# Optimization experiments

Hardware: AMD Instinct MI355X
Metric: run time of the kernel (lower is better)

Reference implementation:

```python
import jax, jax.numpy as jnp
import numpy as np

B, F, D_IN, H, HEADS, NC = 2048, 64, 32, 128, 4, 16
EPG = 128            # random intra-graph edges per graph
N = B * F            # 131072 nodes
E = B * EPG          # 262144 edges (self-loops added in reference, like PyG GATConv)
LRELU_ATT = 0.2      # PyG GATConv negative_slope
LRELU_CLS = 0.01     # nn.LeakyReLU default


def setup_inputs() -> dict:
    key = jax.random.key(0)
    ks = jax.random.split(key, 24)
    emb = jax.random.normal(ks[0], (B, F, D_IN), jnp.float32)
    # per-graph random connectivity, offset so graphs are disjoint
    src_l = jax.random.randint(ks[1], (B, EPG), 0, F)
    tgt_l = jax.random.randint(ks[2], (B, EPG), 0, F)
    off = (jnp.arange(B) * F)[:, None]
    edge_index = jnp.stack([(src_l + off).reshape(-1), (tgt_l + off).reshape(-1)]).astype(jnp.int32)
    batch_idx = jnp.repeat(jnp.arange(B), F).astype(jnp.int32)
    s = 0.05
    return {
        'emb': emb, 'edge_index': edge_index, 'batch_idx': batch_idx,
        # fused aligner (single unique dim 32)
        'W_align': s * jax.random.normal(ks[3], (D_IN, H), jnp.float32),
        'b_align': jnp.zeros((H,), jnp.float32),
        'gate_logits': jnp.full((F,), 2.2, jnp.float32),
        # GATConv 1: in=H, out=H per head, heads=4, concat
        'W1': s * jax.random.normal(ks[4], (H, HEADS * H), jnp.float32),
        'a_src1': s * jax.random.normal(ks[5], (HEADS, H), jnp.float32),
        'a_dst1': s * jax.random.normal(ks[6], (HEADS, H), jnp.float32),
        'b1': jnp.zeros((HEADS * H,), jnp.float32),
        # GATConv 2: in=HEADS*H, out=H, heads=1, concat=False
        'W2': s * jax.random.normal(ks[7], (HEADS * H, H), jnp.float32),
        'a_src2': s * jax.random.normal(ks[8], (1, H), jnp.float32),
        'a_dst2': s * jax.random.normal(ks[9], (1, H), jnp.float32),
        'b2': jnp.zeros((H,), jnp.float32),
        # classifier MLP
        'Wc1': s * jax.random.normal(ks[10], (H, H // 2), jnp.float32),
        'bc1': jnp.zeros((H // 2,), jnp.float32),
        'Wc2': s * jax.random.normal(ks[11], (H // 2, NC), jnp.float32),
        'bc2': jnp.zeros((NC,), jnp.float32),
    }


def gat_layer(x, src, tgt, W, a_src, a_dst, b, concat):
    heads, dout = a_src.shape
    n = x.shape[0]
    h = (x @ W).reshape(n, heads, dout)                       # [N,h,d]
    e = jax.nn.leaky_relu(jnp.einsum('nhd,hd->nh', h, a_src)[src]
                          + jnp.einsum('nhd,hd->nh', h, a_dst)[tgt], LRELU_ATT)  # [E,h]
    m = jax.ops.segment_max(e, tgt, num_segments=n)           # segment softmax over in-neighbors
    p = jnp.exp(e - m[tgt])
    ssum = jax.ops.segment_sum(p, tgt, num_segments=n)
    alpha = p / (ssum[tgt] + 1e-16)
    out = jax.ops.segment_sum(h[src] * alpha[:, :, None], tgt, num_segments=n)
    out = out.reshape(n, heads * dout) if concat else out.mean(axis=1)
    return out + b


def reference(emb, edge_index, batch_idx, W_align, b_align, gate_logits,
              W1, a_src1, a_dst1, b1, W2, a_src2, a_dst2, b2, Wc1, bc1, Wc2, bc2):
    n = emb.shape[0] * emb.shape[1]
    aligned = emb @ W_align + b_align                         # fused align: [B,F,H]
    gate = jax.nn.sigmoid(gate_logits)                        # [F]
    x = (aligned * gate[None, :, None]).reshape(n, -1)        # gated node features [N,H]
    # add self-loops (GATConv default), eval mode -> dropout is identity
    loops = jnp.arange(n, dtype=edge_index.dtype)
    src = jnp.concatenate([edge_index[0], loops])
    tgt = jnp.concatenate([edge_index[1], loops])
    x = gat_layer(x, src, tgt, W1, a_src1, a_dst1, b1, True)  # [N, 4*H]
    x = jax.nn.elu(x)
    x = gat_layer(x, src, tgt, W2, a_src2, a_dst2, b2, False) # [N, H]
    gsum = jax.ops.segment_sum(x, batch_idx, num_segments=B)  # global_mean_pool
    cnt = jax.ops.segment_sum(jnp.ones((n, 1), x.dtype), batch_idx, num_segments=B)
    g = gsum / cnt                                            # [B, H]
    hc = jax.nn.leaky_relu(g @ Wc1 + bc1, LRELU_CLS)
    logits = hc @ Wc2 + bc2                                   # [B, NC]
    return logits, gate
```

## Files before the change

kernel.cpp:

```cpp
#include <hip/hip_runtime.h>
#include <math.h>

#define BLK 256

constexpr int Bg    = 2048;
constexpr int Fn    = 64;
constexpr int DIN   = 32;
constexpr int Hd    = 128;
constexpr int HEADS = 4;
constexpr int NC    = 16;
constexpr int EPG   = 128;
constexpr int Etot  = Bg * EPG;
constexpr int W1C   = HEADS * Hd;
constexpr int NSTR  = 72;
constexpr int EROW  = 136;
constexpr int PROW  = 72;
constexpr int NE    = EPG + Fn;

typedef __attribute__((ext_vector_type(8))) __bf16 bf16x8;
typedef __attribute__((ext_vector_type(4))) __bf16 bf16x4;
typedef __attribute__((ext_vector_type(4))) float  f32x4;

__device__ __align__(16) __bf16 g_wcombT[W1C * DIN];
__device__ float g_c1[W1C];
__device__ float g_c1s[16];
__device__ __align__(16) __bf16 g_w1F[HEADS*8*64*8];
__device__ __align__(16) __bf16 g_w2F[HEADS*4*8*64*8];
__device__ __align__(16) __bf16 g_wscF[HEADS*4*64*8];
__device__ __align__(16) __bf16 g_bs1F[64*8];

__global__ __launch_bounds__(BLK) void prep1(
    const float* __restrict__ Wa, const float* __restrict__ ba,
    const float* __restrict__ W1)
{
  int i = blockIdx.x * BLK + threadIdx.x;
  if (i < DIN * W1C) {
    int k = i >> 9, n = i & 511;
    float a = 0.f;
    for (int m = 0; m < Hd; ++m) a += Wa[k*Hd + m] * W1[m*W1C + n];
    g_wcombT[n*DIN + k] = (__bf16)a;
  } else if (i < DIN*W1C + W1C) {
    int n = i - DIN*W1C;
    float a = 0.f;
    for (int m = 0; m < Hd; ++m) a += ba[m] * W1[m*W1C + n];
    g_c1[n] = a;
  }
}

constexpr int P2_W2F  = HEADS*4*8*64*8;
constexpr int P2_W1F  = HEADS*8*64*8;
constexpr int P2_WSC  = HEADS*4*64*8;
constexpr int P2_BS1  = 512;
constexpr int P2_TOT  = P2_W2F + P2_W1F + P2_WSC + P2_BS1 + 16;

__global__ __launch_bounds__(BLK) void prep2(
    const float* __restrict__ W2,
    const float* __restrict__ as1, const float* __restrict__ ad1,
    const float* __restrict__ as2, const float* __restrict__ ad2)
{
  int i = blockIdx.x * BLK + threadIdx.x;
  if (i < P2_W2F) {
    int j = i & 7, lane = (i >> 3) & 63, T = i >> 9;
    int hh = T >> 5, Ks = (T >> 3) & 3, Nt = T & 7;
    int q = lane >> 4, l = lane & 15;
    int k = hh*Hd + Ks*32 + q*8 + j;
    int n = Nt*16 + l;
    g_w2F[i] = (__bf16)W2[(size_t)k*Hd + n];
  } else if (i < P2_W2F + P2_W1F) {
    int j = i - P2_W2F;
    int jj = j & 7, lane = (j >> 3) & 63, T = j >> 9;
    int hh = T >> 3, Nt = T & 7;
    int q = lane >> 4, l = lane & 15;
    g_w1F[j] = g_wcombT[(hh*Hd + Nt*16 + l)*DIN + q*8 + jj];
  } else if (i < P2_W2F + P2_W1F + P2_WSC) {
    int j = i - (P2_W2F + P2_W1F);
    int jj = j & 7, lane = (j >> 3) & 63, T = j >> 9;
    int hh = T >> 2, Ks = T & 3;
    int q = lane >> 4, c = lane & 15;
    float a = 0.f;
    if (c < 2) {
      const float* av = c ? ad2 : as2;
      int k = hh*Hd + Ks*32 + q*8 + jj;
      for (int f = 0; f < Hd; ++f) a += W2[(size_t)k*Hd + f] * av[f];
    }
    g_wscF[j] = (__bf16)a;
  } else if (i < P2_W2F + P2_W1F + P2_WSC + P2_BS1) {
    int j = i - (P2_W2F + P2_W1F + P2_WSC);
    int jj = j & 7, lane = j >> 3;
    int q = lane >> 4, c = lane & 15;
    float a = 0.f;
    if (c < 8) {
      int h = c >> 1;
      const float* av = (c & 1) ? (ad1 + h*Hd) : (as1 + h*Hd);
      for (int f = 0; f < Hd; ++f)
        a += (float)g_wcombT[(h*Hd + f)*DIN + q*8 + jj] * av[f];
    }
    g_bs1F[j] = (__bf16)a;
  } else if (i < P2_TOT) {
    int c = i - (P2_W2F + P2_W1F + P2_WSC + P2_BS1);
    float a = 0.f;
    if (c < 8) {
      int h = c >> 1;
      const float* av = (c & 1) ? (ad1 + h*Hd) : (as1 + h*Hd);
      for (int f = 0; f < Hd; ++f) a += g_c1[h*Hd + f] * av[f];
    }
    g_c1s[c] = a;
  }
}

__global__ __launch_bounds__(BLK, 3) void gat_main(
    const float* __restrict__ emb, const int* __restrict__ ei,
    const float* __restrict__ gate_logits,
    const float* __restrict__ b1, const float* __restrict__ b2,
    const float* __restrict__ Wc1, const float* __restrict__ bc1,
    const float* __restrict__ Wc2, const float* __restrict__ bc2,
    float* __restrict__ out)
{
  __shared__ __align__(16) __bf16 hT[Hd * NSTR];
  __shared__ __align__(16) __bf16 eluS[Fn * EROW];
  __shared__ __align__(16) __bf16 Pbf[Fn * PROW];
  __shared__ float sS1s[HEADS][Fn], sS1d[HEADS][Fn];
  __shared__ float sSrc[Fn], sDst[Fn], sSum[Fn], gateS[Fn];
  __shared__ float gpool[Hd], hcS[Fn];
  __shared__ __align__(16) __bf16 wS[Fn];

  unsigned* cells = (unsigned*)eluS;

  const int b    = blockIdx.x;
  const int tid  = threadIdx.x;
  const int lane = tid & 63;
  const int wv   = tid >> 6;
  const int quad = lane >> 4;
  const int l15  = lane & 15;
  const int nodeBase = wv * 16;
  const int m0   = wv * 32;
  const int base = b * Fn;

  const f32x4 zero4 = {0.f, 0.f, 0.f, 0.f};

  int es = 0, et = 0, ecell = 0;
  if (tid < NE) {
    if (tid < EPG) {
      es = ei[(size_t)b*EPG + tid] - base;
      et = ei[(size_t)Etot + (size_t)b*EPG + tid] - base;
    } else {
      es = et = tid - EPG;
    }
    ecell = et * Fn + es;
  }
  #pragma unroll
  for (int i = 0; i < 16; ++i) cells[tid + i*BLK] = 0u;
  {
    float4* p4 = (float4*)Pbf;
    const float4 z4 = {0.f,0.f,0.f,0.f};
    p4[tid] = z4; p4[tid + 256] = z4;
    if (tid < 64) p4[tid + 512] = z4;
  }
  if (tid < Fn) {
    float g = 1.f / (1.f + expf(-gate_logits[tid]));
    gateS[tid] = g; sSum[tid] = 0.f;
    if (b == 0) out[Bg*NC + tid] = g;
  }
  bf16x8 Af;
  {
    const float* ar = emb + ((size_t)base + nodeBase + l15) * DIN + quad * 8;
    float4 e0 = *(const float4*)ar;
    float4 e1 = *(const float4*)(ar + 4);
    Af[0]=(__bf16)e0.x; Af[1]=(__bf16)e0.y; Af[2]=(__bf16)e0.z; Af[3]=(__bf16)e0.w;
    Af[4]=(__bf16)e1.x; Af[5]=(__bf16)e1.y; Af[6]=(__bf16)e1.z; Af[7]=(__bf16)e1.w;
  }
  __syncthreads();

  bool rep = false;
  if (tid < NE) rep = (atomicAdd(&cells[ecell], 1u) == 0u);
  {
    bf16x8 Bs = *(const bf16x8*)(g_bs1F + lane*8);
    f32x4 ds = __builtin_amdgcn_mfma_f32_16x16x32_bf16(Af, Bs, zero4, 0, 0, 0);
    if (l15 < 8) {
      const float cc = g_c1s[l15];
      const int h = l15 >> 1;
      float* dstArr = (l15 & 1) ? &sS1d[h][0] : &sS1s[h][0];
      #pragma unroll
      for (int r = 0; r < 4; ++r) {
        int m = nodeBase + quad*4 + r;
        dstArr[m] = gateS[m] * (ds[r] + cc);
      }
    }
  }
  __syncthreads();

  float fm = 0.f;
  if (tid < NE && rep) fm = (float)cells[ecell];

  float gq[4];
  #pragma unroll
  for (int r = 0; r < 4; ++r) gq[r] = gateS[nodeBase + quad*4 + r];

  f32x4 acc[8];
  #pragma unroll
  for (int i = 0; i < 8; ++i) acc[i] = zero4;
  f32x4 accS = zero4;

  for (int hh = 0; hh < HEADS; ++hh) {
    #pragma unroll
    for (int Nt = 0; Nt < 8; ++Nt) {
      const int n = Nt*16 + l15;
      bf16x8 Bf = *(const bf16x8*)(g_w1F + ((hh*8 + Nt)*64 + lane)*8);
      f32x4 d = __builtin_amdgcn_mfma_f32_16x16x32_bf16(Af, Bf, zero4, 0, 0, 0);
      const float c1v = g_c1[hh*Hd + n];
      bf16x4 hw;
      #pragma unroll
      for (int r = 0; r < 4; ++r) hw[r] = (__bf16)((d[r] + c1v) * gq[r]);
      *(bf16x4*)(hT + n*NSTR + nodeBase + quad*4) = hw;
    }
    if (tid < NE && rep) {
      float e = sS1s[hh][es] + sS1d[hh][et];
      e = (e > 0.f) ? e : 0.2f * e;
      float pe = fm * __expf(e);
      Pbf[et*PROW + es] = (__bf16)pe;
      atomicAdd(&sSum[et], pe);
    }
    __syncthreads();

    {
      bf16x8 Ac[2][2];
      #pragma unroll
      for (int Mi = 0; Mi < 2; ++Mi)
        #pragma unroll
        for (int Ks = 0; Ks < 2; ++Ks)
          Ac[Mi][Ks] = *(const bf16x8*)(hT + (m0 + Mi*16 + l15)*NSTR + Ks*32 + quad*8);
      float4 b1v[2];
      #pragma unroll
      for (int Mi = 0; Mi < 2; ++Mi)
        b1v[Mi] = *(const float4*)&b1[hh*Hd + m0 + Mi*16 + quad*4];
      #pragma unroll
      for (int Nt = 0; Nt < 4; ++Nt) {
        bf16x8 B0 = *(const bf16x8*)(Pbf + (Nt*16 + l15)*PROW + quad*8);
        bf16x8 B1 = *(const bf16x8*)(Pbf + (Nt*16 + l15)*PROW + 32 + quad*8);
        const int t = Nt*16 + l15;
        const float si = 1.f / (sSum[t] + 1e-16f);
        #pragma unroll
        for (int Mi = 0; Mi < 2; ++Mi) {
          f32x4 d = __builtin_amdgcn_mfma_f32_16x16x32_bf16(Ac[Mi][0], B0, zero4, 0, 0, 0);
          d = __builtin_amdgcn_mfma_f32_16x16x32_bf16(Ac[Mi][1], B1, d, 0, 0, 0);
          bf16x4 w;
          #pragma unroll
          for (int r = 0; r < 4; ++r) {
            float hv = d[r]*si + b1v[Mi][r];
            hv = (hv > 0.f) ? hv : (__expf(hv) - 1.f);
            w[r] = (__bf16)hv;
          }
          *(bf16x4*)(eluS + t*EROW + m0 + Mi*16 + quad*4) = w;
        }
      }
    }
    __syncthreads();

    #pragma unroll
    for (int Ks = 0; Ks < 4; ++Ks) {
      bf16x8 A2 = *(const bf16x8*)(eluS + (nodeBase + l15)*EROW + Ks*32 + quad*8);
      #pragma unroll
      for (int Nt = 0; Nt < 8; ++Nt) {
        bf16x8 B2 = *(const bf16x8*)(g_w2F + (((hh*4 + Ks)*8 + Nt)*64 + lane)*8);
        acc[Nt] = __builtin_amdgcn_mfma_f32_16x16x32_bf16(A2, B2, acc[Nt], 0, 0, 0);
      }
      bf16x8 Bs2 = *(const bf16x8*)(g_wscF + ((hh*4 + Ks)*64 + lane)*8);
      accS = __builtin_amdgcn_mfma_f32_16x16x32_bf16(A2, Bs2, accS, 0, 0, 0);
    }
    {
      float4* p4 = (float4*)Pbf;
      const float4 z4 = {0.f,0.f,0.f,0.f};
      p4[tid] = z4; p4[tid + 256] = z4;
      if (tid < 64) p4[tid + 512] = z4;
      if (tid < Fn) sSum[tid] = 0.f;
    }
    __syncthreads();
  }

  #pragma unroll
  for (int Nt = 0; Nt < 8; ++Nt) {
    const int n = Nt*16 + l15;
    bf16x4 hw;
    #pragma unroll
    for (int r = 0; r < 4; ++r) hw[r] = (__bf16)acc[Nt][r];
    *(bf16x4*)(hT + n*NSTR + nodeBase + quad*4) = hw;
  }
  if (l15 == 0) {
    #pragma unroll
    for (int r = 0; r < 4; ++r) sSrc[nodeBase + quad*4 + r] = accS[r];
  } else if (l15 == 1) {
    #pragma unroll
    for (int r = 0; r < 4; ++r) sDst[nodeBase + quad*4 + r] = accS[r];
  }
  __syncthreads();

  if (tid < NE && rep) {
    float e = sSrc[es] + sDst[et];
    e = (e > 0.f) ? e : 0.2f * e;
    float pe = fm * __expf(e);
    Pbf[et*PROW + es] = (__bf16)pe;
    atomicAdd(&sSum[et], pe);
  }
  __syncthreads();

  {
    const int s_ = tid >> 2, part = tid & 3;
    float a = 0.f;
    #pragma unroll
    for (int q = 0; q < 16; ++q) {
      const int t = part*16 + q;
      a += (1.f / (sSum[t] + 1e-16f)) * (float)Pbf[t*PROW + s_];
    }
    a += __shfl_xor(a, 1);
    a += __shfl_xor(a, 2);
    if (part == 0) wS[s_] = (__bf16)(a * (1.f/64.f));
  }
  __syncthreads();

  {
    #pragma unroll
    for (int Mi = 0; Mi < 2; ++Mi) {
      f32x4 d = zero4;
      #pragma unroll
      for (int Ks = 0; Ks < 2; ++Ks) {
        bf16x8 A = *(const bf16x8*)(hT + (m0 + Mi*16 + l15)*NSTR + Ks*32 + quad*8);
        bf16x8 Bw = *(const bf16x8*)(wS + Ks*32 + quad*8);
        d = __builtin_amdgcn_mfma_f32_16x16x32_bf16(A, Bw, d, 0, 0, 0);
      }
      if (l15 == 0) {
        #pragma unroll
        for (int r = 0; r < 4; ++r) {
          const int f = m0 + Mi*16 + quad*4 + r;
          gpool[f] = d[r] + b2[f];
        }
      }
    }
  }
  __syncthreads();

  {
    const int c = tid >> 2, p = tid & 3;
    float a = 0.f;
    #pragma unroll
    for (int i = 0; i < 32; ++i) {
      const int k = p*32 + i;
      a += gpool[k] * Wc1[k*Fn + c];
    }
    a += __shfl_xor(a, 1);
    a += __shfl_xor(a, 2);
    if (p == 0) {
      a += bc1[c];
      hcS[c] = (a > 0.f) ? a : 0.01f * a;
    }
  }
  __syncthreads();

  {
    const int c = tid >> 4, p = tid & 15;
    float a = 0.f;
    #pragma unroll
    for (int i = 0; i < 4; ++i) {
      const int k = p*4 + i;
      a += hcS[k] * Wc2[k*NC + c];
    }
    a += __shfl_xor(a, 1);
    a += __shfl_xor(a, 2);
    a += __shfl_xor(a, 4);
    a += __shfl_xor(a, 8);
    if (p == 0) out[b*NC + c] = a + bc2[c];
  }
}

extern "C" void kernel_launch(void* const* d_in, const int* in_sizes, int n_in,
                              void* d_out, int out_size, void* d_ws, size_t ws_size,
                              hipStream_t stream) {
  const float* emb = (const float*)d_in[0];
  const int*   ei  = (const int*)  d_in[1];
  const float* Wa  = (const float*)d_in[3];
  const float* ba  = (const float*)d_in[4];
  const float* gl  = (const float*)d_in[5];
  const float* W1  = (const float*)d_in[6];
  const float* as1 = (const float*)d_in[7];
  const float* ad1 = (const float*)d_in[8];
  const float* b1  = (const float*)d_in[9];
  const float* W2  = (const float*)d_in[10];
  const float* as2 = (const float*)d_in[11];
  const float* ad2 = (const float*)d_in[12];
  const float* b2  = (const float*)d_in[13];
  const float* Wc1 = (const float*)d_in[14];
  const float* bc1 = (const float*)d_in[15];
  const float* Wc2 = (const float*)d_in[16];
  const float* bc2 = (const float*)d_in[17];
  float* out = (float*)d_out;

  const int prep1N = DIN*W1C + W1C;
  hipLaunchKernelGGL(prep1, dim3((prep1N + BLK - 1)/BLK), dim3(BLK), 0, stream,
                     Wa, ba, W1);
  hipLaunchKernelGGL(prep2, dim3((P2_TOT + BLK - 1)/BLK), dim3(BLK), 0, stream,
                     W2, as1, ad1, as2, ad2);
  hipLaunchKernelGGL(gat_main, dim3(Bg), dim3(BLK), 0, stream,
                     emb, ei, gl, b1, b2, Wc1, bc1, Wc2, bc2, out);
}
```

Measured before the change: 197.1 us.

## Shrink LDS row strides and parallelize weight-prep kernels with coalesced loads

Reduces the hT and Pbf row padding from 72 to 68 bf16, which shrinks shared memory per block and changes the LDS bank mapping for the MFMA operand reads. The prep kernels are restructured. prep1 stages W_align in LDS and writes coalesced output. prep2 scatters W2 from coalesced reads, and splits the attention-projection dot products across lanes with shuffle reductions and unrolled partial sums. The smaller stride may raise occupancy or cut bank conflicts, but 16-byte vector loads at stride 68 need alignment care. The prep kernels are a small part of total time.

```diff
diff --git a/kernel.cpp b/kernel.cpp
--- a/kernel.cpp
+++ b/kernel.cpp
@@ -12,9 +12,9 @@
 constexpr int EPG   = 128;
 constexpr int Etot  = Bg * EPG;
 constexpr int W1C   = HEADS * Hd;
-constexpr int NSTR  = 72;
+constexpr int NSTR  = 68;
 constexpr int EROW  = 136;
-constexpr int PROW  = 72;
+constexpr int PROW  = 68;
 constexpr int NE    = EPG + Fn;
 
 typedef __attribute__((ext_vector_type(8))) __bf16 bf16x8;
@@ -33,25 +33,54 @@
     const float* __restrict__ Wa, const float* __restrict__ ba,
     const float* __restrict__ W1)
 {
-  int i = blockIdx.x * BLK + threadIdx.x;
+  __shared__ float WaS[DIN * Hd];
+  const int tid = threadIdx.x;
+  for (int i = tid; i < DIN * Hd; i += BLK) {
+    int k = i >> 7, m = i & 127;
+    WaS[m * DIN + k] = Wa[i];
+  }
+  __syncthreads();
+
+  int i = blockIdx.x * BLK + tid;
   if (i < DIN * W1C) {
-    int k = i >> 9, n = i & 511;
-    float a = 0.f;
-    for (int m = 0; m < Hd; ++m) a += Wa[k*Hd + m] * W1[m*W1C + n];
-    g_wcombT[n*DIN + k] = (__bf16)a;
+    int k = i & 31, n = i >> 5;
+    float a0 = 0.f, a1 = 0.f, a2 = 0.f, a3 = 0.f;
+    #pragma unroll
+    for (int m = 0; m < Hd; m += 4) {
+      a0 += WaS[(m  )*DIN + k] * W1[(m  )*W1C + n];
+      a1 += WaS[(m+1)*DIN + k] * W1[(m+1)*W1C + n];
+      a2 += WaS[(m+2)*DIN + k] * W1[(m+2)*W1C + n];
+      a3 += WaS[(m+3)*DIN + k] * W1[(m+3)*W1C + n];
+    }
+    g_wcombT[i] = (__bf16)(a0 + a1 + a2 + a3);
   } else if (i < DIN*W1C + W1C) {
     int n = i - DIN*W1C;
-    float a = 0.f;
-    for (int m = 0; m < Hd; ++m) a += ba[m] * W1[m*W1C + n];
-    g_c1[n] = a;
+    float a0 = 0.f, a1 = 0.f, a2 = 0.f, a3 = 0.f;
+    #pragma unroll
+    for (int m = 0; m < Hd; m += 4) {
+      a0 += ba[m  ] * W1[(m  )*W1C + n];
+      a1 += ba[m+1] * W1[(m+1)*W1C + n];
+      a2 += ba[m+2] * W1[(m+2)*W1C + n];
+      a3 += ba[m+3] * W1[(m+3)*W1C + n];
+    }
+    g_c1[n] = a0 + a1 + a2 + a3;
   }
 }
 
-constexpr int P2_W2F  = HEADS*4*8*64*8;
-constexpr int P2_W1F  = HEADS*8*64*8;
-constexpr int P2_WSC  = HEADS*4*64*8;
-constexpr int P2_BS1  = 512;
-constexpr int P2_TOT  = P2_W2F + P2_W1F + P2_WSC + P2_BS1 + 16;
+constexpr int R_W2F  = 65536;
+constexpr int R_W1F  = 16384;
+constexpr int R_WSCZ = 8192;
+constexpr int R_WSCD = 4096;
+constexpr int R_BS1Z = 512;
+constexpr int R_BS1D = 1024;
+constexpr int R_C1S  = 128;
+constexpr int B0 = R_W2F;
+constexpr int B1 = B0 + R_W1F;
+constexpr int B2 = B1 + R_WSCZ;
+constexpr int B3 = B2 + R_WSCD;
+constexpr int B4 = B3 + R_BS1Z;
+constexpr int B5 = B4 + R_BS1D;
+constexpr int P2_TOT = B5 + R_C1S;
 
 __global__ __launch_bounds__(BLK) void prep2(
     const float* __restrict__ W2,
@@ -59,52 +88,84 @@
     const float* __restrict__ as2, const float* __restrict__ ad2)
 {
   int i = blockIdx.x * BLK + threadIdx.x;
-  if (i < P2_W2F) {
-    int j = i & 7, lane = (i >> 3) & 63, T = i >> 9;
-    int hh = T >> 5, Ks = (T >> 3) & 3, Nt = T & 7;
-    int q = lane >> 4, l = lane & 15;
-    int k = hh*Hd + Ks*32 + q*8 + j;
-    int n = Nt*16 + l;
-    g_w2F[i] = (__bf16)W2[(size_t)k*Hd + n];
-  } else if (i < P2_W2F + P2_W1F) {
-    int j = i - P2_W2F;
+  if (i < B0) {
+    int k = i >> 7, n = i & 127;
+    int hh = k >> 7, Ks = (k >> 5) & 3, q = (k >> 3) & 3, j = k & 7;
+    int Nt = n >> 4, l = n & 15;
+    int idx = (((hh*4 + Ks)*8 + Nt)*64 + (q*16 + l))*8 + j;
+    g_w2F[idx] = (__bf16)W2[i];
+  } else if (i < B1) {
+    int j = i - B0;
     int jj = j & 7, lane = (j >> 3) & 63, T = j >> 9;
     int hh = T >> 3, Nt = T & 7;
     int q = lane >> 4, l = lane & 15;
     g_w1F[j] = g_wcombT[(hh*Hd + Nt*16 + l)*DIN + q*8 + jj];
-  } else if (i < P2_W2F + P2_W1F + P2_WSC) {
-    int j = i - (P2_W2F + P2_W1F);
-    int jj = j & 7, lane = (j >> 3) & 63, T = j >> 9;
-    int hh = T >> 2, Ks = T & 3;
-    int q = lane >> 4, c = lane & 15;
-    float a = 0.f;
-    if (c < 2) {
-      const float* av = c ? ad2 : as2;
-      int k = hh*Hd + Ks*32 + q*8 + jj;
-      for (int f = 0; f < Hd; ++f) a += W2[(size_t)k*Hd + f] * av[f];
-    }
-    g_wscF[j] = (__bf16)a;
-  } else if (i < P2_W2F + P2_W1F + P2_WSC + P2_BS1) {
-    int j = i - (P2_W2F + P2_W1F + P2_WSC);
-    int jj = j & 7, lane = j >> 3;
-    int q = lane >> 4, c = lane & 15;
+  } else if (i < B2) {
+    int j = i - B1;
+    int lane = (j >> 3) & 63, c = lane & 15;
+    if (c >= 2) g_wscF[j] = (__bf16)0.f;
+  } else if (i < B3) {
+    int j = i - B2;
+    int p = j & 3, c = (j >> 2) & 1, k = j >> 3;
+    const float* av = c ? ad2 : as2;
+    float a0 = 0.f, a1 = 0.f, a2 = 0.f, a3 = 0.f;
+    #pragma unroll
+    for (int q = 0; q < 32; q += 4) {
+      int f = p*32 + q;
+      a0 += W2[(size_t)k*Hd + f    ] * av[f    ];
+      a1 += W2[(size_t)k*Hd + f + 1] * av[f + 1];
+      a2 += W2[(size_t)k*Hd + f + 2] * av[f + 2];
+      a3 += W2[(size_t)k*Hd + f + 3] * av[f + 3];
+    }
+    float a = a0 + a1 + a2 + a3;
+    a += __shfl_xor(a, 1);
+    a += __shfl_xor(a, 2);
+    if (p == 0) {
+      int T = k >> 5, q2 = (k >> 3) & 3, jj = k & 7;
+      g_wscF[(T*64 + q2*16 + c)*8 + jj] = (__bf16)a;
+    }
+  } else if (i < B4) {
+    int j = i - B3;
+    int lane = j >> 3, c = lane & 15;
+    if (c >= 8) g_bs1F[j] = (__bf16)0.f;
+  } else if (i < B5) {
+    int j = i - B4;
+    int p = j & 3, c = (j >> 2) & 7, kk = j >> 5;
+    int h = c >> 1;
+    const float* av = (c & 1) ? (ad1 + h*Hd) : (as1 + h*Hd);
+    float a0 = 0.f, a1 = 0.f, a2 = 0.f, a3 = 0.f;
+    #pragma unroll
+    for (int q = 0; q < 32; q += 4) {
+      int f = p*32 + q;
+      a0 += (float)g_wcombT[(h*Hd + f    )*DIN + kk] * av[f    ];
+      a1 += (float)g_wcombT[(h*Hd + f + 1)*DIN + kk] * av[f + 1];
+      a2 += (float)g_wcombT[(h*Hd + f + 2)*DIN + kk] * av[f + 2];
+      a3 += (float)g_wcombT[(h*Hd + f + 3)*DIN + kk] * av[f + 3];
+    }
+    float a = a0 + a1 + a2 + a3;
+    a += __shfl_xor(a, 1);
+    a += __shfl_xor(a, 2);
+    if (p == 0) {
+      int q2 = kk >> 3, jj = kk & 7;
+      g_bs1F[(q2*16 + c)*8 + jj] = (__bf16)a;
+    }
+  } else if (i < P2_TOT) {
+    int j = i - B5;
+    int p = j & 7, c = j >> 3;
     float a = 0.f;
     if (c < 8) {
       int h = c >> 1;
       const float* av = (c & 1) ? (ad1 + h*Hd) : (as1 + h*Hd);
-      for (int f = 0; f < Hd; ++f)
-        a += (float)g_wcombT[(h*Hd + f)*DIN + q*8 + jj] * av[f];
-    }
-    g_bs1F[j] = (__bf16)a;
-  } else if (i < P2_TOT) {
-    int c = i - (P2_W2F + P2_W1F + P2_WSC + P2_BS1);
-    float a = 0.f;
-    if (c < 8) {
-      int h = c >> 1;
-      const float* av = (c & 1) ? (ad1 + h*Hd) : (as1 + h*Hd);
-      for (int f = 0; f < Hd; ++f) a += g_c1[h*Hd + f] * av[f];
-    }
-    g_c1s[c] = a;
+      #pragma unroll
+      for (int q = 0; q < 16; ++q) {
+        int f = p*16 + q;
+        a += g_c1[h*Hd + f] * av[f];
+      }
+    }
+    a += __shfl_xor(a, 1);
+    a += __shfl_xor(a, 2);
+    a += __shfl_xor(a, 4);
+    if (p == 0) g_c1s[c] = a;
   }
 }
 
@@ -154,7 +215,7 @@
     float4* p4 = (float4*)Pbf;
     const float4 z4 = {0.f,0.f,0.f,0.f};
     p4[tid] = z4; p4[tid + 256] = z4;
-    if (tid < 64) p4[tid + 512] = z4;
+    if (tid < 32) p4[tid + 512] = z4;
   }
   if (tid < Fn) {
     float g = 1.f / (1.f + expf(-gate_logits[tid]));
@@ -235,14 +296,14 @@
         b1v[Mi] = *(const float4*)&b1[hh*Hd + m0 + Mi*16 + quad*4];
       #pragma unroll
       for (int Nt = 0; Nt < 4; ++Nt) {
-        bf16x8 B0 = *(const bf16x8*)(Pbf + (Nt*16 + l15)*PROW + quad*8);
-        bf16x8 B1 = *(const bf16x8*)(Pbf + (Nt*16 + l15)*PROW + 32 + quad*8);
+        bf16x8 B0f = *(const bf16x8*)(Pbf + (Nt*16 + l15)*PROW + quad*8);
+        bf16x8 B1f = *(const bf16x8*)(Pbf + (Nt*16 + l15)*PROW + 32 + quad*8);
         const int t = Nt*16 + l15;
         const float si = 1.f / (sSum[t] + 1e-16f);
         #pragma unroll
         for (int Mi = 0; Mi < 2; ++Mi) {
-          f32x4 d = __builtin_amdgcn_mfma_f32_16x16x32_bf16(Ac[Mi][0], B0, zero4, 0, 0, 0);
-          d = __builtin_amdgcn_mfma_f32_16x16x32_bf16(Ac[Mi][1], B1, d, 0, 0, 0);
+          f32x4 d = __builtin_amdgcn_mfma_f32_16x16x32_bf16(Ac[Mi][0], B0f, zero4, 0, 0, 0);
+          d = __builtin_amdgcn_mfma_f32_16x16x32_bf16(Ac[Mi][1], B1f, d, 0, 0, 0);
           bf16x4 w;
           #pragma unroll
           for (int r = 0; r < 4; ++r) {
@@ -271,7 +332,7 @@
       float4* p4 = (float4*)Pbf;
       const float4 z4 = {0.f,0.f,0.f,0.f};
       p4[tid] = z4; p4[tid + 256] = z4;
-      if (tid < 64) p4[tid + 512] = z4;
+      if (tid < 32) p4[tid + 512] = z4;
       if (tid < Fn) sSum[tid] = 0.f;
     }
     __syncthreads();
```

After: 190.4 us. 1.04x faster.
